# Optimization experiments

Measured on AMD Instinct MI355X. Metric: run time of the kernel, lower is better.

Reference implementation:

```python
import jax, jax.numpy as jnp
import numpy as np

B, C_IN, T = 8, 1024, 4096
D_VQ, K, DS = 1024, 2048, 2


def setup_inputs() -> dict:
    key = jax.random.key(0)
    k1, k2, k3, k4 = jax.random.split(key, 4)
    x = jax.random.normal(k1, (B, C_IN, T), dtype=jnp.float32)
    x_mask = jnp.ones((B, 1, T), dtype=jnp.float32)
    conv_in_w = jax.random.normal(k2, (D_VQ, C_IN, DS), dtype=jnp.float32) * 0.02
    conv_in_b = jnp.zeros((D_VQ,), dtype=jnp.float32)
    codebook = jax.random.normal(k3, (K, D_VQ), dtype=jnp.float32)
    conv_out_w = jax.random.normal(k4, (C_IN, D_VQ), dtype=jnp.float32) * 0.02
    conv_out_b = jnp.zeros((C_IN,), dtype=jnp.float32)
    return {"x": x, "x_mask": x_mask, "conv_in_w": conv_in_w,
            "conv_in_b": conv_in_b, "codebook": codebook,
            "conv_out_w": conv_out_w, "conv_out_b": conv_out_b}


def reference(x, x_mask, conv_in_w, conv_in_b, codebook, conv_out_w, conv_out_b):
    x_len = x.shape[2]  # 4096, divisible by DS=2 -> no padding branch
    # conv_in: Conv1d(C_IN -> D_VQ, kernel=DS, stride=DS)
    h = jax.lax.conv_general_dilated(
        x, conv_in_w, window_strides=(DS,), padding='VALID',
        dimension_numbers=('NCH', 'OIH', 'NCH')) + conv_in_b[None, :, None]
    xt = h.transpose(0, 2, 1)  # [B, T', D]
    # euclidean VQ: squared distances to codebook, argmin assignment
    d2 = (jnp.sum(xt * xt, -1, keepdims=True)
          - 2.0 * jnp.einsum('btd,kd->btk', xt, codebook)
          + jnp.sum(codebook * codebook, -1))  # [B, T', K]
    idx = jnp.argmin(d2, axis=-1)  # [B, T'] int
    quant = codebook[idx]  # [B, T', D]
    # commitment loss (EMA codebook: codebook detached)
    loss = jnp.mean(jnp.square(xt - jax.lax.stop_gradient(quant)))
    # straight-through estimator
    q = xt + jax.lax.stop_gradient(quant - xt)
    qc = q.transpose(0, 2, 1)  # [B, D, T']
    # conv_out: nearest upsample by DS, then 1x1 conv
    up = jnp.repeat(qc, DS, axis=-1)  # [B, D, T]
    out = jnp.einsum('od,bdt->bot', conv_out_w, up) + conv_out_b[None, :, None]
    out = (out * x_mask)[:, :, :x_len]
    indices = idx[:, None, :]  # 'b t -> b 1 t'
    return out, indices, loss
```

## Files before the change

kernel.cpp:

```cpp
#include <hip/hip_runtime.h>

#define NB   8
#define CIN  1024
#define TT   4096
#define DVQ  1024
#define KC   2048
#define MM   16384

typedef short s16x8 __attribute__((ext_vector_type(8)));
typedef float f32x4 __attribute__((ext_vector_type(4)));

__device__ __forceinline__ short f2bf(float f) {
    unsigned u = __float_as_uint(f);
    u = u + 0x7fffu + ((u >> 16) & 1u);
    return (short)(u >> 16);
}
__device__ __forceinline__ float bf2f(short h) {
    return __uint_as_float(((unsigned)(unsigned short)h) << 16);
}
__device__ __forceinline__ unsigned pk(short a, short b) {
    return (unsigned)(unsigned short)a | ((unsigned)(unsigned short)b << 16);
}
__device__ __forceinline__ void split3(float v, short& h, short& m, short& l) {
    h = f2bf(v); float r1 = v - bf2f(h);
    m = f2bf(r1); float r2 = r1 - bf2f(m);
    l = f2bf(r2);
}
__device__ __forceinline__ int aswz(int row, int q) {
    return row * 40 + (((q ^ (row >> 3)) & 3) << 3);
}
__device__ __forceinline__ bool lesskey(float v, int k, float v2, int k2) {
    return v < v2 || (v == v2 && k < k2);
}
__device__ __forceinline__ void merge2(float& b1, int& k1, float& b2, int& k2,
                                       float o1, int ok1, float o2, int ok2) {
    if (lesskey(o1, ok1, b1, k1)) {
        float nb2; int nk2;
        if (lesskey(b1, k1, o2, ok2)) { nb2 = b1; nk2 = k1; } else { nb2 = o2; nk2 = ok2; }
        b1 = o1; k1 = ok1; b2 = nb2; k2 = nk2;
    } else if (lesskey(o1, ok1, b2, k2)) {
        b2 = o1; k2 = ok1;
    }
}

__global__ __launch_bounds__(256) void k_split3(const float* __restrict__ src,
                                                short* __restrict__ h, short* __restrict__ m,
                                                short* __restrict__ l, int n4) {
    int i = blockIdx.x * 256 + threadIdx.x;
    if (i >= n4) return;
    float4 v = ((const float4*)src)[i];
    short4 H, M, L;
    split3(v.x, H.x, M.x, L.x); split3(v.y, H.y, M.y, L.y);
    split3(v.z, H.z, M.z, L.z); split3(v.w, H.w, M.w, L.w);
    ((short4*)h)[i] = H; ((short4*)m)[i] = M; ((short4*)l)[i] = L;
}

__global__ __launch_bounds__(256) void k_split2(const float* __restrict__ src,
                                                short* __restrict__ h, short* __restrict__ l, int n4) {
    int i = blockIdx.x * 256 + threadIdx.x;
    if (i >= n4) return;
    float4 v = ((const float4*)src)[i];
    short4 H, L;
    H.x = f2bf(v.x); L.x = f2bf(v.x - bf2f(H.x));
    H.y = f2bf(v.y); L.y = f2bf(v.y - bf2f(H.y));
    H.z = f2bf(v.z); L.z = f2bf(v.z - bf2f(H.z));
    H.w = f2bf(v.w); L.w = f2bf(v.w - bf2f(H.w));
    ((short4*)h)[i] = H; ((short4*)l)[i] = L;
}

__global__ __launch_bounds__(256) void k_cnorm(const float* __restrict__ cb,
                                               float* __restrict__ c32,
                                               double* __restrict__ c64) {
    __shared__ double red[256];
    const float* row = cb + (size_t)blockIdx.x * DVQ;
    float4 v = ((const float4*)row)[threadIdx.x];
    red[threadIdx.x] = (double)v.x * v.x + (double)v.y * v.y +
                       (double)v.z * v.z + (double)v.w * v.w;
    __syncthreads();
    for (int o = 128; o > 0; o >>= 1) {
        if (threadIdx.x < o) red[threadIdx.x] += red[threadIdx.x + o];
        __syncthreads();
    }
    if (threadIdx.x == 0) { c64[blockIdx.x] = red[0]; c32[blockIdx.x] = (float)red[0]; }
}

__global__ __launch_bounds__(256, 2) void k_conv(const float* __restrict__ x,
                                                 const short* __restrict__ wh,
                                                 const short* __restrict__ wm,
                                                 const short* __restrict__ wl,
                                                 const float* __restrict__ bias,
                                                 float* __restrict__ xt,
                                                 short* __restrict__ xth,
                                                 short* __restrict__ xtl) {
    __shared__ short sAh[128 * 40], sAm[128 * 40], sAl[128 * 40];
    __shared__ short sBh[64 * 40],  sBm[64 * 40],  sBl[64 * 40];
    const int tid = threadIdx.x;
    const int lin = blockIdx.x;
    const int cx = lin & 7, j = lin >> 3;
    const int m0 = (cx * 16 + (j >> 4)) * 128;
    const int n0 = (j & 15) * 64;
    const int b = m0 >> 11, t0 = m0 & 2047;
    const float* xb = x + (size_t)b * CIN * TT + 2 * t0;

    const int aw = tid >> 6, p = tid & 63;
    const int brow = tid >> 2, bq = tid & 3;
    const int ln = tid & 15, quad = (tid >> 4) & 3;
    const int r0 = (aw >> 1) * 64, c0 = (aw & 1) * 32;

    f32x4 acc[4][2], sums[4][2];
#pragma unroll
    for (int r = 0; r < 4; ++r)
#pragma unroll
        for (int c = 0; c < 2; ++c) { acc[r][c] = 0.f; sums[r][c] = 0.f; }

    float4 av[4];
    uint4 bh0, bm0, bl0;
#pragma unroll
    for (int r = 0; r < 4; ++r) av[r] = *(const float4*)(xb + (size_t)(4 * r + aw) * TT + 4 * p);
    {
        const size_t o = (size_t)(n0 + brow) * 2048 + bq * 8;
        bh0 = *(const uint4*)&wh[o]; bm0 = *(const uint4*)&wm[o]; bl0 = *(const uint4*)&wl[o];
    }

    for (int it = 0; it < 64; ++it) {
        __syncthreads();
#pragma unroll
        for (int r = 0; r < 4; ++r) {
            const int ii = r * 4 + aw;
            const int q = ii >> 2, off = (2 * ii) & 7;
            const int a0 = aswz(2 * p, q) + off;
            const int a1 = aswz(2 * p + 1, q) + off;
            float4 v = av[r];
            short hx, mx, lx, hy, my, ly;
            split3(v.x, hx, mx, lx); split3(v.y, hy, my, ly);
            *(unsigned*)&sAh[a0] = pk(hx, hy);
            *(unsigned*)&sAm[a0] = pk(mx, my);
            *(unsigned*)&sAl[a0] = pk(lx, ly);
            split3(v.z, hx, mx, lx); split3(v.w, hy, my, ly);
            *(unsigned*)&sAh[a1] = pk(hx, hy);
            *(unsigned*)&sAm[a1] = pk(mx, my);
            *(unsigned*)&sAl[a1] = pk(lx, ly);
        }
        {
            const int w0 = brow * 40 + bq * 8;
            *(uint4*)&sBh[w0] = bh0; *(uint4*)&sBm[w0] = bm0; *(uint4*)&sBl[w0] = bl0;
        }
        __syncthreads();
        if (it + 1 < 64) {
            const int i0 = (it + 1) * 16, k0 = (it + 1) * 32;
#pragma unroll
            for (int r = 0; r < 4; ++r)
                av[r] = *(const float4*)(xb + (size_t)(i0 + 4 * r + aw) * TT + 4 * p);
            const size_t o = (size_t)(n0 + brow) * 2048 + k0 + bq * 8;
            bh0 = *(const uint4*)&wh[o]; bm0 = *(const uint4*)&wm[o]; bl0 = *(const uint4*)&wl[o];
        }
        s16x8 fah[4], fam[4], fal[4];
#pragma unroll
        for (int r = 0; r < 4; ++r) {
            const int base = aswz(r0 + r * 16 + ln, quad);
            fah[r] = *(const s16x8*)&sAh[base];
            fam[r] = *(const s16x8*)&sAm[base];
            fal[r] = *(const s16x8*)&sAl[base];
        }
#pragma unroll
        for (int c = 0; c < 2; ++c) {
            const int bb = (c0 + c * 16 + ln) * 40 + quad * 8;
            s16x8 fbh = *(const s16x8*)&sBh[bb];
            s16x8 fbm = *(const s16x8*)&sBm[bb];
            s16x8 fbl = *(const s16x8*)&sBl[bb];
#pragma unroll
            for (int r = 0; r < 4; ++r) {
                acc[r][c] = __builtin_amdgcn_mfma_f32_16x16x32_bf16(fah[r], fbh, acc[r][c], 0, 0, 0);
                acc[r][c] = __builtin_amdgcn_mfma_f32_16x16x32_bf16(fah[r], fbm, acc[r][c], 0, 0, 0);
                acc[r][c] = __builtin_amdgcn_mfma_f32_16x16x32_bf16(fam[r], fbh, acc[r][c], 0, 0, 0);
                acc[r][c] = __builtin_amdgcn_mfma_f32_16x16x32_bf16(fah[r], fbl, acc[r][c], 0, 0, 0);
                acc[r][c] = __builtin_amdgcn_mfma_f32_16x16x32_bf16(fam[r], fbm, acc[r][c], 0, 0, 0);
                acc[r][c] = __builtin_amdgcn_mfma_f32_16x16x32_bf16(fal[r], fbh, acc[r][c], 0, 0, 0);
            }
        }
        if (it & 1) {
#pragma unroll
            for (int r = 0; r < 4; ++r)
#pragma unroll
                for (int c = 0; c < 2; ++c) { sums[r][c] += acc[r][c]; acc[r][c] = 0.f; }
        }
    }
#pragma unroll
    for (int c = 0; c < 2; ++c) {
        const int n = n0 + c0 + c * 16 + ln;
        const float bv = bias[n];
#pragma unroll
        for (int r = 0; r < 4; ++r)
#pragma unroll
            for (int g = 0; g < 4; ++g) {
                const int m = m0 + r0 + r * 16 + quad * 4 + g;
                const float v = sums[r][c][g] + bv;
                const size_t o = (size_t)m * DVQ + n;
                xt[o] = v;
                short h = f2bf(v);
                xth[o] = h;
                xtl[o] = f2bf(v - bf2f(h));
            }
    }
}

__global__ __launch_bounds__(256, 2) void k_dot(const short* __restrict__ xth,
                                                const short* __restrict__ xtl,
                                                const short* __restrict__ cbh,
                                                const short* __restrict__ cbl,
                                                const float* __restrict__ c32,
                                                float4* __restrict__ pb) {
    __shared__ __align__(16) short sAh[128 * 40], sAl[128 * 40], sBh[128 * 40], sBl[128 * 40];
    const int tid = threadIdx.x;
    const int n0 = blockIdx.x * 128, m0 = blockIdx.y * 128;
    const int ar = tid >> 2, q = tid & 3, kk = q * 8;
    const int ln = tid & 15, quad = (tid >> 4) & 3, wv = tid >> 6;
    const int r0 = (wv >> 1) * 64, c0 = (wv & 1) * 64;

    f32x4 acc[4][4];
#pragma unroll
    for (int r = 0; r < 4; ++r)
#pragma unroll
        for (int c = 0; c < 4; ++c) acc[r][c] = 0.f;

    uint4 a0 = *(const uint4*)&xth[(size_t)(m0 + ar) * 1024 + kk];
    uint4 a1 = *(const uint4*)&xth[(size_t)(m0 + 64 + ar) * 1024 + kk];
    uint4 a2 = *(const uint4*)&xtl[(size_t)(m0 + ar) * 1024 + kk];
    uint4 a3 = *(const uint4*)&xtl[(size_t)(m0 + 64 + ar) * 1024 + kk];
    uint4 b0 = *(const uint4*)&cbh[(size_t)(n0 + ar) * 1024 + kk];
    uint4 b1 = *(const uint4*)&cbh[(size_t)(n0 + 64 + ar) * 1024 + kk];
    uint4 b2 = *(const uint4*)&cbl[(size_t)(n0 + ar) * 1024 + kk];
    uint4 b3 = *(const uint4*)&cbl[(size_t)(n0 + 64 + ar) * 1024 + kk];

    for (int it = 0; it < 32; ++it) {
        __syncthreads();
        *(uint4*)&sAh[aswz(ar, q)] = a0;
        *(uint4*)&sAh[aswz(64 + ar, q)] = a1;
        *(uint4*)&sAl[aswz(ar, q)] = a2;
        *(uint4*)&sAl[aswz(64 + ar, q)] = a3;
        {
            const int w0 = ar * 40 + kk, w1 = (64 + ar) * 40 + kk;
            *(uint4*)&sBh[w0] = b0; *(uint4*)&sBh[w1] = b1;
            *(uint4*)&sBl[w0] = b2; *(uint4*)&sBl[w1] = b3;
        }
        __syncthreads();
        if (it + 1 < 32) {
            const int k0 = (it + 1) * 32;
            a0 = *(const uint4*)&xth[(size_t)(m0 + ar) * 1024 + k0 + kk];
            a1 = *(const uint4*)&xth[(size_t)(m0 + 64 + ar) * 1024 + k0 + kk];
            a2 = *(const uint4*)&xtl[(size_t)(m0 + ar) * 1024 + k0 + kk];
            a3 = *(const uint4*)&xtl[(size_t)(m0 + 64 + ar) * 1024 + k0 + kk];
            b0 = *(const uint4*)&cbh[(size_t)(n0 + ar) * 1024 + k0 + kk];
            b1 = *(const uint4*)&cbh[(size_t)(n0 + 64 + ar) * 1024 + k0 + kk];
            b2 = *(const uint4*)&cbl[(size_t)(n0 + ar) * 1024 + k0 + kk];
            b3 = *(const uint4*)&cbl[(size_t)(n0 + 64 + ar) * 1024 + k0 + kk];
        }
        s16x8 fah[4], fal[4];
#pragma unroll
        for (int r = 0; r < 4; ++r) {
            const int base = aswz(r0 + r * 16 + ln, quad);
            fah[r] = *(const s16x8*)&sAh[base];
            fal[r] = *(const s16x8*)&sAl[base];
        }
#pragma unroll
        for (int c = 0; c < 4; ++c) {
            const int bb = (c0 + c * 16 + ln) * 40 + quad * 8;
            s16x8 fbh = *(const s16x8*)&sBh[bb];
            s16x8 fbl = *(const s16x8*)&sBl[bb];
#pragma unroll
            for (int r = 0; r < 4; ++r) {
                acc[r][c] = __builtin_amdgcn_mfma_f32_16x16x32_bf16(fah[r], fbh, acc[r][c], 0, 0, 0);
                acc[r][c] = __builtin_amdgcn_mfma_f32_16x16x32_bf16(fah[r], fbl, acc[r][c], 0, 0, 0);
                acc[r][c] = __builtin_amdgcn_mfma_f32_16x16x32_bf16(fal[r], fbh, acc[r][c], 0, 0, 0);
            }
        }
    }
    float tb1[16], tb2[16]; int tk1[16], tk2[16];
#pragma unroll
    for (int i = 0; i < 16; ++i) { tb1[i] = INFINITY; tb2[i] = INFINITY; tk1[i] = 0; tk2[i] = 0; }
#pragma unroll
    for (int c = 0; c < 4; ++c) {
        const int n = n0 + c0 + c * 16 + ln;
        const float cn = c32[n];
#pragma unroll
        for (int r = 0; r < 4; ++r)
#pragma unroll
            for (int g = 0; g < 4; ++g) {
                const float s = cn - 2.0f * acc[r][c][g];
                const int i = r * 4 + g;
                if (s < tb1[i]) { tb2[i] = tb1[i]; tk2[i] = tk1[i]; tb1[i] = s; tk1[i] = n; }
                else if (s < tb2[i]) { tb2[i] = s; tk2[i] = n; }
            }
    }
#pragma unroll
    for (int off = 1; off < 16; off <<= 1) {
#pragma unroll
        for (int i = 0; i < 16; ++i) {
            float o1 = __shfl_xor(tb1[i], off); int ok1 = __shfl_xor(tk1[i], off);
            float o2 = __shfl_xor(tb2[i], off); int ok2 = __shfl_xor(tk2[i], off);
            merge2(tb1[i], tk1[i], tb2[i], tk2[i], o1, ok1, o2, ok2);
        }
    }
    __syncthreads();
    float4* part = (float4*)sAh;
    if (ln == 0) {
#pragma unroll
        for (int i = 0; i < 16; ++i) {
            const int lr = (i >> 2) * 16 + quad * 4 + (i & 3);
            float4 v; v.x = tb1[i]; v.y = tb2[i];
            v.z = __int_as_float(tk1[i]); v.w = __int_as_float(tk2[i]);
            part[wv * 64 + lr] = v;
        }
    }
    __syncthreads();
    if (tid < 128) {
        const int row = tid, h = row >> 6, lr = row & 63;
        float4 A = part[(2 * h) * 64 + lr];
        float4 B = part[(2 * h + 1) * 64 + lr];
        float b1v = A.x, b2v = A.y; int k1 = __float_as_int(A.z), k2 = __float_as_int(A.w);
        merge2(b1v, k1, b2v, k2, B.x, __float_as_int(B.z), B.y, __float_as_int(B.w));
        float4 o; o.x = b1v; o.y = b2v; o.z = __int_as_float(k1); o.w = __int_as_float(k2);
        pb[(size_t)blockIdx.x * MM + m0 + row] = o;
    }
}

__global__ __launch_bounds__(256) void k_pick(const float4* __restrict__ pb,
                                              const double* __restrict__ c64,
                                              const float* __restrict__ xt,
                                              const float* __restrict__ cb,
                                              int* __restrict__ idxbuf,
                                              float* __restrict__ idx_out) {
    const int wv = threadIdx.x >> 6, lane = threadIdx.x & 63;
    const int m = blockIdx.x * 4 + wv;
    float4 P = pb[m];
    float b1 = P.x, b2 = P.y; int k1 = __float_as_int(P.z), k2 = __float_as_int(P.w);
#pragma unroll
    for (int s = 1; s < 16; ++s) {
        float4 Q = pb[(size_t)s * MM + m];
        merge2(b1, k1, b2, k2, Q.x, __float_as_int(Q.z), Q.y, __float_as_int(Q.w));
    }
    const float* xr = xt + (size_t)m * DVQ;
    const float* c1 = cb + (size_t)k1 * DVQ;
    const float* c2 = cb + (size_t)k2 * DVQ;
    double e1 = 0.0, e2 = 0.0;
    for (int j = 0; j < DVQ / 64; ++j) {
        const int d = j * 64 + lane;
        const double xv = xr[d];
        e1 += xv * (double)c1[d]; e2 += xv * (double)c2[d];
    }
    for (int off = 32; off > 0; off >>= 1) { e1 += __shfl_xor(e1, off); e2 += __shfl_xor(e2, off); }
    if (lane == 0) {
        const double s1 = c64[k1] - 2.0 * e1;
        const double s2 = c64[k2] - 2.0 * e2;
        const int kf = (s2 < s1 || (s2 == s1 && k2 < k1)) ? k2 : k1;
        idxbuf[m] = kf;
        idx_out[m] = (float)kf;
    }
}

__global__ __launch_bounds__(256) void k_losspart(const float* __restrict__ xt,
                                                  const float* __restrict__ cb,
                                                  const int* __restrict__ idxbuf,
                                                  float* __restrict__ partials) {
    __shared__ float red[256];
    const int m = blockIdx.x;
    const int row = idxbuf[m];
    float4 a = ((const float4*)(xt + (size_t)m * DVQ))[threadIdx.x];
    float4 c = ((const float4*)(cb + (size_t)row * DVQ))[threadIdx.x];
    const float dx = a.x - c.x, dy = a.y - c.y, dz = a.z - c.z, dw = a.w - c.w;
    red[threadIdx.x] = dx * dx + dy * dy + dz * dz + dw * dw;
    __syncthreads();
    for (int o = 128; o > 0; o >>= 1) {
        if (threadIdx.x < o) red[threadIdx.x] += red[threadIdx.x + o];
        __syncthreads();
    }
    if (threadIdx.x == 0) partials[m] = red[0];
}

__global__ __launch_bounds__(256) void k_lossfinal(const float* __restrict__ partials,
                                                   float* __restrict__ loss_out) {
    __shared__ float red[256];
    float s = 0.0f;
    for (int i = threadIdx.x; i < MM; i += 256) s += partials[i];
    red[threadIdx.x] = s;
    __syncthreads();
    for (int o = 128; o > 0; o >>= 1) {
        if (threadIdx.x < o) red[threadIdx.x] += red[threadIdx.x + o];
        __syncthreads();
    }
    if (threadIdx.x == 0) loss_out[0] = red[0] / (float)((size_t)MM * DVQ);
}

__global__ __launch_bounds__(256, 2) void k_out(const int* __restrict__ idxbuf,
                                                const short* __restrict__ ch,
                                                const short* __restrict__ cl,
                                                const short* __restrict__ wh,
                                                const short* __restrict__ wl,
                                                const float* __restrict__ bias,
                                                const float* __restrict__ xm,
                                                float* __restrict__ outp) {
    __shared__ short sAh[128 * 40], sAl[128 * 40], sBh[128 * 40], sBl[128 * 40];
    __shared__ int rows_s[128];
    const int tid = threadIdx.x;
    const int m0 = blockIdx.y * 128, n0 = blockIdx.x * 128;
    if (tid < 128) rows_s[tid] = idxbuf[m0 + tid];
    __syncthreads();
    const int ar = tid >> 2, q = tid & 3, kk = q * 8;
    const int ln = tid & 15, quad = (tid >> 4) & 3, wv = tid >> 6;
    const int r0 = (wv >> 1) * 64, c0 = (wv & 1) * 64;
    const size_t ra0 = (size_t)rows_s[ar] * 1024, ra1 = (size_t)rows_s[64 + ar] * 1024;

    f32x4 acc[4][4];
#pragma unroll
    for (int r = 0; r < 4; ++r)
#pragma unroll
        for (int c = 0; c < 4; ++c) acc[r][c] = 0.f;

    uint4 a0 = *(const uint4*)&ch[ra0 + kk];
    uint4 a1 = *(const uint4*)&ch[ra1 + kk];
    uint4 a2 = *(const uint4*)&cl[ra0 + kk];
    uint4 a3 = *(const uint4*)&cl[ra1 + kk];
    uint4 b0 = *(const uint4*)&wh[(size_t)(n0 + ar) * 1024 + kk];
    uint4 b1 = *(const uint4*)&wh[(size_t)(n0 + 64 + ar) * 1024 + kk];
    uint4 b2 = *(const uint4*)&wl[(size_t)(n0 + ar) * 1024 + kk];
    uint4 b3 = *(const uint4*)&wl[(size_t)(n0 + 64 + ar) * 1024 + kk];

    for (int it = 0; it < 32; ++it) {
        __syncthreads();
        *(uint4*)&sAh[aswz(ar, q)] = a0;
        *(uint4*)&sAh[aswz(64 + ar, q)] = a1;
        *(uint4*)&sAl[aswz(ar, q)] = a2;
        *(uint4*)&sAl[aswz(64 + ar, q)] = a3;
        {
            const int w0 = ar * 40 + kk, w1 = (64 + ar) * 40 + kk;
            *(uint4*)&sBh[w0] = b0; *(uint4*)&sBh[w1] = b1;
            *(uint4*)&sBl[w0] = b2; *(uint4*)&sBl[w1] = b3;
        }
        __syncthreads();
        if (it + 1 < 32) {
            const int k0 = (it + 1) * 32;
            a0 = *(const uint4*)&ch[ra0 + k0 + kk];
            a1 = *(const uint4*)&ch[ra1 + k0 + kk];
            a2 = *(const uint4*)&cl[ra0 + k0 + kk];
            a3 = *(const uint4*)&cl[ra1 + k0 + kk];
            b0 = *(const uint4*)&wh[(size_t)(n0 + ar) * 1024 + k0 + kk];
            b1 = *(const uint4*)&wh[(size_t)(n0 + 64 + ar) * 1024 + k0 + kk];
            b2 = *(const uint4*)&wl[(size_t)(n0 + ar) * 1024 + k0 + kk];
            b3 = *(const uint4*)&wl[(size_t)(n0 + 64 + ar) * 1024 + k0 + kk];
        }
        s16x8 fah[4], fal[4];
#pragma unroll
        for (int r = 0; r < 4; ++r) {
            const int base = aswz(r0 + r * 16 + ln, quad);
            fah[r] = *(const s16x8*)&sAh[base];
            fal[r] = *(const s16x8*)&sAl[base];
        }
#pragma unroll
        for (int c = 0; c < 4; ++c) {
            const int bb = (c0 + c * 16 + ln) * 40 + quad * 8;
            s16x8 fbh = *(const s16x8*)&sBh[bb];
            s16x8 fbl = *(const s16x8*)&sBl[bb];
#pragma unroll
            for (int r = 0; r < 4; ++r) {
                acc[r][c] = __builtin_amdgcn_mfma_f32_16x16x32_bf16(fah[r], fbh, acc[r][c], 0, 0, 0);
                acc[r][c] = __builtin_amdgcn_mfma_f32_16x16x32_bf16(fah[r], fbl, acc[r][c], 0, 0, 0);
                acc[r][c] = __builtin_amdgcn_mfma_f32_16x16x32_bf16(fal[r], fbh, acc[r][c], 0, 0, 0);
            }
        }
    }
#pragma unroll
    for (int c = 0; c < 4; ++c) {
        const int n = n0 + c0 + c * 16 + ln;
        const float bv = bias[n];
#pragma unroll
        for (int r = 0; r < 4; ++r)
#pragma unroll
            for (int g = 0; g < 4; ++g) {
                const int m = m0 + r0 + r * 16 + quad * 4 + g;
                const int b = m >> 11, t = m & 2047;
                const float mk0 = xm[(size_t)b * TT + 2 * t];
                const float mk1 = xm[(size_t)b * TT + 2 * t + 1];
                const float v = acc[r][c][g] + bv;
                float2 o2; o2.x = v * mk0; o2.y = v * mk1;
                *(float2*)&outp[((size_t)b * CIN + n) * TT + 2 * t] = o2;
            }
    }
}

extern "C" void kernel_launch(void* const* d_in, const int* in_sizes, int n_in,
                              void* d_out, int out_size, void* d_ws, size_t ws_size,
                              hipStream_t stream) {
    const float* x  = (const float*)d_in[0];
    const float* xm = (const float*)d_in[1];
    const float* wi = (const float*)d_in[2];
    const float* bi = (const float*)d_in[3];
    const float* cb = (const float*)d_in[4];
    const float* wo = (const float*)d_in[5];
    const float* bo = (const float*)d_in[6];

    float* outp     = (float*)d_out;
    float* idx_out  = outp + (size_t)NB * CIN * TT;
    float* loss_out = idx_out + MM;
    float* xt  = outp;
    short* xth = (short*)(outp + 16777216);
    short* xtl = xth + 16777216;

    char* p = (char*)d_ws;
    short* wih = (short*)p; p += (size_t)CIN * 2048 * 2;
    short* wim = (short*)p; p += (size_t)CIN * 2048 * 2;
    short* wil = (short*)p; p += (size_t)CIN * 2048 * 2;
    short* cbh = (short*)p; p += (size_t)KC * DVQ * 2;
    short* cbl = (short*)p; p += (size_t)KC * DVQ * 2;
    short* woh = (short*)p; p += (size_t)CIN * DVQ * 2;
    short* wol = (short*)p; p += (size_t)CIN * DVQ * 2;
    float*  c32 = (float*)p;  p += KC * sizeof(float);
    double* c64 = (double*)p; p += KC * sizeof(double);
    float4* pb  = (float4*)p; p += (size_t)16 * MM * sizeof(float4);
    float* partials = (float*)p; p += MM * sizeof(float);
    int*   idxbuf   = (int*)p;

    dim3 blk(256);
    k_split3<<<dim3(2048), blk, 0, stream>>>(wi, wih, wim, wil, CIN * 2048 / 4);
    k_split2<<<dim3(2048), blk, 0, stream>>>(cb, cbh, cbl, KC * DVQ / 4);
    k_split2<<<dim3(1024), blk, 0, stream>>>(wo, woh, wol, CIN * DVQ / 4);
    k_cnorm <<<dim3(KC),   blk, 0, stream>>>(cb, c32, c64);
    k_conv  <<<dim3(2048), blk, 0, stream>>>(x, wih, wim, wil, bi, xt, xth, xtl);
    k_dot   <<<dim3(16, 128), blk, 0, stream>>>(xth, xtl, cbh, cbl, c32, pb);
    k_pick  <<<dim3(MM / 4), blk, 0, stream>>>(pb, c64, xt, cb, idxbuf, idx_out);
    k_losspart<<<dim3(MM), blk, 0, stream>>>(xt, cb, idxbuf, partials);
    k_lossfinal<<<1, blk, 0, stream>>>(partials, loss_out);
    k_out   <<<dim3(8, 128), blk, 0, stream>>>(idxbuf, cbh, cbl, woh, wol, bo, xm, outp);
}
```

Before: 1.146 ms.

## Pre-split and transpose conv input into bf16 planes, use async LDS-load GEMM

```diff
diff --git a/kernel.cpp b/kernel.cpp
--- a/kernel.cpp
+++ b/kernel.cpp
@@ -41,6 +41,10 @@
     } else if (lesskey(o1, ok1, b2, k2)) {
         b2 = o1; k2 = ok1;
     }
+}
+__device__ __forceinline__ void gload16(void* lds, const void* g) {
+    __builtin_amdgcn_global_load_lds((const __attribute__((address_space(1))) void*)g,
+                                     (__attribute__((address_space(3))) void*)lds, 16, 0, 0);
 }
 
 __global__ __launch_bounds__(256) void k_split3(const float* __restrict__ src,
@@ -82,6 +86,134 @@
         __syncthreads();
     }
     if (threadIdx.x == 0) { c64[blockIdx.x] = red[0]; c32[blockIdx.x] = (float)red[0]; }
+}
+
+__global__ __launch_bounds__(256) void k_asplit(const float* __restrict__ x,
+                                                short* __restrict__ ah,
+                                                short* __restrict__ am,
+                                                short* __restrict__ al) {
+    const int bid = blockIdx.x;
+    const int b = bid >> 7, cblk = (bid >> 5) & 3, tch = bid & 31;
+    const int c = cblk * 256 + threadIdx.x;
+    const float* xr = x + ((size_t)b * CIN + c) * TT + tch * 128;
+    unsigned* AH = (unsigned*)ah;
+    unsigned* AM = (unsigned*)am;
+    unsigned* AL = (unsigned*)al;
+    const int mbase = b * 2048 + tch * 64;
+#pragma unroll 4
+    for (int i = 0; i < 32; ++i) {
+        float4 v = *(const float4*)(xr + 4 * i);
+        short h0, mm0, l0, h1, mm1, l1, h2, mm2, l2, h3, mm3, l3;
+        split3(v.x, h0, mm0, l0); split3(v.y, h1, mm1, l1);
+        split3(v.z, h2, mm2, l2); split3(v.w, h3, mm3, l3);
+        const size_t o0 = (size_t)(mbase + 2 * i) * 1024 + c;
+        const size_t o1 = o0 + 1024;
+        AH[o0] = pk(h0, h1); AM[o0] = pk(mm0, mm1); AL[o0] = pk(l0, l1);
+        AH[o1] = pk(h2, h3); AM[o1] = pk(mm2, mm3); AL[o1] = pk(l2, l3);
+    }
+}
+
+__global__ __launch_bounds__(256, 2) void k_convp(const short* __restrict__ ah,
+                                                  const short* __restrict__ am,
+                                                  const short* __restrict__ al,
+                                                  const short* __restrict__ wh,
+                                                  const short* __restrict__ wm,
+                                                  const short* __restrict__ wl,
+                                                  const float* __restrict__ bias,
+                                                  float* __restrict__ xt,
+                                                  short* __restrict__ xth,
+                                                  short* __restrict__ xtl) {
+    __shared__ short s[6][128 * 32];
+    const int tid = threadIdx.x;
+    const int lin = blockIdx.x;
+    const int cx = lin & 7, j = lin >> 3;
+    const int m0 = (cx * 16 + (j >> 3)) * 128;
+    const int n0 = (j & 7) * 128;
+
+    const int wv = tid >> 6, lane = tid & 63;
+    const int slot0 = wv * 128 + lane, slot1 = slot0 + 64;
+    const int row0 = slot0 >> 2, c80 = (slot0 & 3) * 8;
+    const int row1 = slot1 >> 2, c81 = (slot1 & 3) * 8;
+    const size_t ga0 = (size_t)(m0 + row0) * 2048 + c80;
+    const size_t ga1 = (size_t)(m0 + row1) * 2048 + c81;
+    const size_t gb0 = (size_t)(n0 + row0) * 2048 + c80;
+    const size_t gb1 = (size_t)(n0 + row1) * 2048 + c81;
+
+    const int ln = tid & 15, quad = (tid >> 4) & 3;
+    const int r0w = (wv >> 1) * 64, c0w = (wv & 1) * 64;
+
+    f32x4 acc[4][4], sums[4][4];
+#pragma unroll
+    for (int r = 0; r < 4; ++r)
+#pragma unroll
+        for (int c = 0; c < 4; ++c) { acc[r][c] = 0.f; sums[r][c] = 0.f; }
+
+#pragma unroll 2
+    for (int it = 0; it < 64; ++it) {
+        const int k0 = it * 32;
+        __syncthreads();
+        gload16(&s[0][slot0 * 8], ah + ga0 + k0);
+        gload16(&s[0][slot1 * 8], ah + ga1 + k0);
+        gload16(&s[1][slot0 * 8], am + ga0 + k0);
+        gload16(&s[1][slot1 * 8], am + ga1 + k0);
+        gload16(&s[2][slot0 * 8], al + ga0 + k0);
+        gload16(&s[2][slot1 * 8], al + ga1 + k0);
+        gload16(&s[3][slot0 * 8], wh + gb0 + k0);
+        gload16(&s[3][slot1 * 8], wh + gb1 + k0);
+        gload16(&s[4][slot0 * 8], wm + gb0 + k0);
+        gload16(&s[4][slot1 * 8], wm + gb1 + k0);
+        gload16(&s[5][slot0 * 8], wl + gb0 + k0);
+        gload16(&s[5][slot1 * 8], wl + gb1 + k0);
+        __syncthreads();
+
+        s16x8 fa0[4], fa1[4], fa2[4];
+#pragma unroll
+        for (int r = 0; r < 4; ++r) {
+            const int off = (r0w + r * 16 + ln) * 32 + quad * 8;
+            fa0[r] = *(const s16x8*)&s[0][off];
+            fa1[r] = *(const s16x8*)&s[1][off];
+            fa2[r] = *(const s16x8*)&s[2][off];
+        }
+#pragma unroll
+        for (int c = 0; c < 4; ++c) {
+            const int boff = (c0w + c * 16 + ln) * 32 + quad * 8;
+            s16x8 fbh = *(const s16x8*)&s[3][boff];
+            s16x8 fbm = *(const s16x8*)&s[4][boff];
+            s16x8 fbl = *(const s16x8*)&s[5][boff];
+#pragma unroll
+            for (int r = 0; r < 4; ++r) {
+                acc[r][c] = __builtin_amdgcn_mfma_f32_16x16x32_bf16(fa0[r], fbh, acc[r][c], 0, 0, 0);
+                acc[r][c] = __builtin_amdgcn_mfma_f32_16x16x32_bf16(fa0[r], fbm, acc[r][c], 0, 0, 0);
+                acc[r][c] = __builtin_amdgcn_mfma_f32_16x16x32_bf16(fa1[r], fbh, acc[r][c], 0, 0, 0);
+                acc[r][c] = __builtin_amdgcn_mfma_f32_16x16x32_bf16(fa0[r], fbl, acc[r][c], 0, 0, 0);
+                acc[r][c] = __builtin_amdgcn_mfma_f32_16x16x32_bf16(fa1[r], fbm, acc[r][c], 0, 0, 0);
+                acc[r][c] = __builtin_amdgcn_mfma_f32_16x16x32_bf16(fa2[r], fbh, acc[r][c], 0, 0, 0);
+            }
+        }
+        if (it & 1) {
+#pragma unroll
+            for (int r = 0; r < 4; ++r)
+#pragma unroll
+                for (int c = 0; c < 4; ++c) { sums[r][c] += acc[r][c]; acc[r][c] = 0.f; }
+        }
+    }
+#pragma unroll
+    for (int c = 0; c < 4; ++c) {
+        const int n = n0 + c0w + c * 16 + ln;
+        const float bv = bias[n];
+#pragma unroll
+        for (int r = 0; r < 4; ++r)
+#pragma unroll
+            for (int g = 0; g < 4; ++g) {
+                const int m = m0 + r0w + r * 16 + quad * 4 + g;
+                const float v = sums[r][c][g] + bv;
+                const size_t o = (size_t)m * DVQ + n;
+                xt[o] = v;
+                short h = f2bf(v);
+                xth[o] = h;
+                xtl[o] = f2bf(v - bf2f(h));
+            }
+    }
 }
 
 __global__ __launch_bounds__(256, 2) void k_conv(const float* __restrict__ x,
@@ -517,14 +649,24 @@
     double* c64 = (double*)p; p += KC * sizeof(double);
     float4* pb  = (float4*)p; p += (size_t)16 * MM * sizeof(float4);
     float* partials = (float*)p; p += MM * sizeof(float);
-    int*   idxbuf   = (int*)p;
+    int*   idxbuf   = (int*)p;   p += MM * sizeof(int);
+    short* Ah = (short*)p; p += (size_t)MM * 2048 * 2;
+    short* Am = (short*)p; p += (size_t)MM * 2048 * 2;
+    short* Al = (short*)p; p += (size_t)MM * 2048 * 2;
+    const size_t need = (size_t)(p - (char*)d_ws);
+    const bool fast = ws_size >= need;
 
     dim3 blk(256);
     k_split3<<<dim3(2048), blk, 0, stream>>>(wi, wih, wim, wil, CIN * 2048 / 4);
     k_split2<<<dim3(2048), blk, 0, stream>>>(cb, cbh, cbl, KC * DVQ / 4);
     k_split2<<<dim3(1024), blk, 0, stream>>>(wo, woh, wol, CIN * DVQ / 4);
     k_cnorm <<<dim3(KC),   blk, 0, stream>>>(cb, c32, c64);
-    k_conv  <<<dim3(2048), blk, 0, stream>>>(x, wih, wim, wil, bi, xt, xth, xtl);
+    if (fast) {
+        k_asplit<<<dim3(1024), blk, 0, stream>>>(x, Ah, Am, Al);
+        k_convp <<<dim3(1024), blk, 0, stream>>>(Ah, Am, Al, wih, wim, wil, bi, xt, xth, xtl);
+    } else {
+        k_conv  <<<dim3(2048), blk, 0, stream>>>(x, wih, wim, wil, bi, xt, xth, xtl);
+    }
     k_dot   <<<dim3(16, 128), blk, 0, stream>>>(xth, xtl, cbh, cbl, c32, pb);
     k_pick  <<<dim3(MM / 4), blk, 0, stream>>>(pb, c64, xt, cb, idxbuf, idx_out);
     k_losspart<<<dim3(MM), blk, 0, stream>>>(xt, cb, idxbuf, partials);
```

New measurement: 1.081 ms. 1.06x faster.
